# Performance work log

Hardware: AMD Instinct MI355X
Metric: run time of the kernel (lower is better)

## Reference

```python
import jax, jax.numpy as jnp
import numpy as np

D_MODEL = 512
D_INNER = 1024   # expand=2
D_STATE = 16
D_CONV = 4
DT_RANK = 32     # ceil(d_model/16)
B, L = 2, 2048


def _params(kbase):
    kk = jax.random.split(kbase, 9)
    n = lambda k, s, sc: jax.random.normal(k, s, jnp.float32) * sc
    return dict(
        Win=n(kk[0], (2 * D_INNER, D_MODEL), D_MODEL ** -0.5),
        convw=n(kk[1], (D_INNER, 1, D_CONV), 0.2),
        convb=n(kk[2], (D_INNER,), 0.02),
        Wx=n(kk[3], (DT_RANK + 2 * D_STATE, D_INNER), D_INNER ** -0.5),
        Wdt=n(kk[4], (D_INNER, DT_RANK), DT_RANK ** -0.5),
        dtb=n(kk[5], (D_INNER,), 0.1),
        Alog=n(kk[6], (D_INNER, D_STATE), 0.5),
        Dp=n(kk[7], (D_INNER,), 1.0),
        Wout=n(kk[8], (D_MODEL, D_INNER), D_INNER ** -0.5),
    )


def setup_inputs() -> dict:
    key = jax.random.key(0)
    k0, kf, kr = jax.random.split(key, 3)
    inp = {"hidden_states": jax.random.normal(k0, (B, L, D_MODEL), jnp.float32)}
    for name, v in _params(kf).items():
        inp[name + "_f"] = v
    for name, v in _params(kr).items():
        inp[name + "_r"] = v
    return inp


def _mamba(x, Win, convw, convb, Wx, Wdt, dtb, Alog, Dp, Wout):
    # x: (B, L, D_MODEL)
    Bb = x.shape[0]
    xz = jnp.einsum('bld,ed->ble', x, Win)            # (B, L, 2*D_INNER)
    xs, z = jnp.split(xz, 2, axis=-1)
    # causal depthwise conv over length
    xc = jnp.swapaxes(xs, 1, 2)                       # (B, D_INNER, L)
    xc = jax.lax.conv_general_dilated(
        xc, convw, (1,), [(D_CONV - 1, 0)], feature_group_count=D_INNER)
    xs = jax.nn.silu(jnp.swapaxes(xc + convb[None, :, None], 1, 2))  # (B, L, D_INNER)
    # input-dependent SSM params
    x_dbl = jnp.einsum('bld,ed->ble', xs, Wx)         # (B, L, DT_RANK+2*D_STATE)
    dt = x_dbl[..., :DT_RANK]
    Bm = x_dbl[..., DT_RANK:DT_RANK + D_STATE]        # (B, L, D_STATE)
    Cm = x_dbl[..., DT_RANK + D_STATE:]               # (B, L, D_STATE)
    dt = jax.nn.softplus(jnp.einsum('blr,dr->bld', dt, Wdt) + dtb)   # (B, L, D_INNER)
    A = -jnp.exp(Alog)                                # (D_INNER, D_STATE), strictly negative
    dA = jnp.exp(dt[..., None] * A)                   # (B, L, D_INNER, D_STATE)
    dBu = dt[..., None] * Bm[:, :, None, :] * xs[..., None]

    def step(h, inp):
        dA_t, dBu_t, C_t = inp
        h = dA_t * h + dBu_t                          # (B, D_INNER, D_STATE)
        return h, jnp.einsum('bds,bs->bd', h, C_t)

    h0 = jnp.zeros((Bb, D_INNER, D_STATE), x.dtype)
    _, ys = jax.lax.scan(
        step, h0,
        (jnp.moveaxis(dA, 1, 0), jnp.moveaxis(dBu, 1, 0), jnp.moveaxis(Cm, 1, 0)))
    y = jnp.moveaxis(ys, 0, 1) + xs * Dp              # (B, L, D_INNER)
    y = y * jax.nn.silu(z)                            # gated output
    return jnp.einsum('bld,ed->ble', y, Wout)         # (B, L, D_MODEL)


def reference(hidden_states,
              Win_f, convw_f, convb_f, Wx_f, Wdt_f, dtb_f, Alog_f, Dp_f, Wout_f,
              Win_r, convw_r, convb_r, Wx_r, Wdt_r, dtb_r, Alog_r, Dp_r, Wout_r):
    out_f = _mamba(hidden_states, Win_f, convw_f, convb_f, Wx_f, Wdt_f, dtb_f,
                   Alog_f, Dp_f, Wout_f)
    out_r = _mamba(hidden_states[:, ::-1, :], Win_r, convw_r, convb_r, Wx_r,
                   Wdt_r, dtb_r, Alog_r, Dp_r, Wout_r)[:, ::-1, :]
    return out_f + out_r  # bidirectional_strategy == 'add'
```

## Files before the change

### kernel.cpp

```cpp
#include <hip/hip_runtime.h>
#include <cmath>

#define B_   2
#define L_   2048
#define DM_  512
#define DI_  1024
#define DS_  16
#define DTR_ 32
#define M_   (B_*L_)
#define NC_  64
#define CL_  32
#define KS_  8
#define LOG2E_ 1.44269504088896340736f
#define LN2_   0.69314718055994530942f

typedef __attribute__((ext_vector_type(8))) short short8;
typedef __attribute__((ext_vector_type(4))) float floatx4;

__device__ inline unsigned short f2bf(float f) {
  unsigned u = __float_as_uint(f);
  unsigned r = (u + 0x7fffu + ((u >> 16) & 1u)) >> 16;
  return (unsigned short)r;
}
__device__ inline float bf2f(unsigned short u) {
  return __uint_as_float(((unsigned)u) << 16);
}
__device__ inline unsigned short f2h(float f) {
  _Float16 h = (_Float16)f;
  return *(unsigned short*)&h;
}
__device__ inline float h2f(unsigned short u) {
  _Float16 h = *(_Float16*)&u;
  return (float)h;
}
__device__ inline float fexp2(float x) { return __builtin_amdgcn_exp2f(x); }
__device__ inline float flog2(float x) { return __builtin_amdgcn_logf(x); }

__device__ inline void gload_lds16(const unsigned short* g, unsigned short* l) {
  __builtin_amdgcn_global_load_lds(
      (const __attribute__((address_space(1))) void*)g,
      (__attribute__((address_space(3))) void*)l, 16, 0, 0);
}

__global__ __launch_bounds__(256) void gemm1_mfma_k(
    const unsigned short* __restrict__ A,
    const unsigned short* __restrict__ Wf, const unsigned short* __restrict__ Wr,
    unsigned short* __restrict__ Cf, unsigned short* __restrict__ Cr,
    int M, int N, int K)
{
  __shared__ unsigned short At[2][128 * 32];
  __shared__ unsigned short Wt[2][128 * 32];
  const unsigned short* W = blockIdx.z ? Wr : Wf;
  unsigned short* C = blockIdx.z ? Cr : Cf;
  const int tid  = threadIdx.x;
  const int w    = tid >> 6;
  const int lane = tid & 63;
  const int wm   = w >> 1, wn = w & 1;
  const int row0 = blockIdx.y * 128, col0 = blockIdx.x * 128;
  const int lrow  = lane >> 2;
  const int lkoff = (lane & 3) * 8;
  const int fr = lane & 15;
  const int fq = (lane >> 4) * 8;

  floatx4 acc[4][4];
#pragma unroll
  for (int i = 0; i < 4; ++i)
#pragma unroll
    for (int j = 0; j < 4; ++j)
#pragma unroll
      for (int r = 0; r < 4; ++r) acc[i][j][r] = 0.f;

  auto stage = [&](int buf, int k0) {
#pragma unroll
    for (int j = 0; j < 2; ++j) {
      int r = w * 32 + j * 16;
      gload_lds16(A + (size_t)(row0 + r + lrow) * K + k0 + lkoff, At[buf] + r * 32);
      gload_lds16(W + (size_t)(col0 + r + lrow) * K + k0 + lkoff, Wt[buf] + r * 32);
    }
  };
  auto compute = [&](int buf) {
    short8 af[4], bf[4];
#pragma unroll
    for (int i = 0; i < 4; ++i) {
      af[i] = *(const short8*)&At[buf][(64 * wm + 16 * i + fr) * 32 + fq];
      bf[i] = *(const short8*)&Wt[buf][(64 * wn + 16 * i + fr) * 32 + fq];
    }
#pragma unroll
    for (int i = 0; i < 4; ++i)
#pragma unroll
      for (int j = 0; j < 4; ++j)
        acc[i][j] = __builtin_amdgcn_mfma_f32_16x16x32_bf16(af[i], bf[j], acc[i][j], 0, 0, 0);
  };

  const int NT = K >> 5;
  stage(0, 0);
  __syncthreads();
  int cur = 0;
  for (int t = 0; t < NT - 1; ++t) {
    stage(cur ^ 1, (t + 1) << 5);
    compute(cur);
    __syncthreads();
    cur ^= 1;
  }
  compute(cur);

#pragma unroll
  for (int i = 0; i < 4; ++i) {
    int rg = row0 + 64 * wm + 16 * i + ((lane >> 4) << 2);
#pragma unroll
    for (int j = 0; j < 4; ++j) {
      int cg = col0 + 64 * wn + 16 * j + (lane & 15);
#pragma unroll
      for (int r = 0; r < 4; ++r)
        C[(size_t)(rg + r) * N + cg] = f2bf(acc[i][j][r]);
    }
  }
}

__global__ __launch_bounds__(256) void gemm4_fused_k(
    const unsigned short* __restrict__ ybf, const unsigned short* __restrict__ Woutbf,
    const unsigned short* __restrict__ ybr, const unsigned short* __restrict__ Woutbr,
    float* __restrict__ out)
{
  __shared__ unsigned short At[2][2][64 * 32];
  __shared__ unsigned short Wt[2][2][64 * 32];
  const int tid  = threadIdx.x;
  const int w    = tid >> 6;
  const int lane = tid & 63;
  const int col0 = blockIdx.x * 64;
  const int row0 = blockIdx.y * 64;
  const int lrow  = lane >> 2;
  const int lkoff = (lane & 3) * 8;
  const int fr = lane & 15;
  const int fq = (lane >> 4) * 8;

  floatx4 acc[4];
#pragma unroll
  for (int j = 0; j < 4; ++j)
#pragma unroll
    for (int r = 0; r < 4; ++r) acc[j][r] = 0.f;

  auto stage = [&](int buf, int t) {
    const unsigned short* A = (t & 16) ? ybr : ybf;
    const unsigned short* W = (t & 16) ? Woutbr : Woutbf;
    const int k0 = (t & 15) << 6;
#pragma unroll
    for (int h = 0; h < 2; ++h) {
      gload_lds16(A + (size_t)(row0 + 16 * w + lrow) * DI_ + k0 + 32 * h + lkoff,
                  At[buf][h] + (16 * w) * 32);
      gload_lds16(W + (size_t)(col0 + 16 * w + lrow) * DI_ + k0 + 32 * h + lkoff,
                  Wt[buf][h] + (16 * w) * 32);
    }
  };
  auto compute = [&](int buf) {
    short8 af[2], bf[2][4];
#pragma unroll
    for (int h = 0; h < 2; ++h) {
      af[h] = *(const short8*)&At[buf][h][(16 * w + fr) * 32 + fq];
#pragma unroll
      for (int j = 0; j < 4; ++j)
        bf[h][j] = *(const short8*)&Wt[buf][h][(16 * j + fr) * 32 + fq];
    }
#pragma unroll
    for (int h = 0; h < 2; ++h)
#pragma unroll
      for (int j = 0; j < 4; ++j)
        acc[j] = __builtin_amdgcn_mfma_f32_16x16x32_bf16(af[h], bf[h][j], acc[j], 0, 0, 0);
  };

  stage(0, 0);
  __syncthreads();
  int cur = 0;
  for (int t = 0; t < 31; ++t) {
    stage(cur ^ 1, t + 1);
    compute(cur);
    __syncthreads();
    cur ^= 1;
  }
  compute(cur);

  const int rg = row0 + 16 * w + ((lane >> 4) << 2);
#pragma unroll
  for (int j = 0; j < 4; ++j) {
    int cg = col0 + 16 * j + (lane & 15);
#pragma unroll
    for (int r = 0; r < 4; ++r)
      out[(size_t)(rg + r) * DM_ + cg] = acc[j][r];
  }
}

__global__ __launch_bounds__(256) void gemm2_mfma_k(
    const unsigned short* __restrict__ xsbf, const unsigned short* __restrict__ xsbr,
    const unsigned short* __restrict__ Wxbf, const unsigned short* __restrict__ Wxbr,
    float* __restrict__ part)
{
  __shared__ unsigned short At[2][128 * 32];
  __shared__ unsigned short Wt[2][64 * 32];
  const int tid  = threadIdx.x;
  const int w    = tid >> 6;
  const int lane = tid & 63;
  const int ks   = blockIdx.x;
  const int row0 = blockIdx.y * 128;
  const int dir  = blockIdx.z;
  const unsigned short* A = dir ? xsbr : xsbf;
  const unsigned short* W = dir ? Wxbr : Wxbf;
  const int kbase = ks * (DI_ / KS_);
  const int lrow  = lane >> 2;
  const int lkoff = (lane & 3) * 8;
  const int fr = lane & 15;
  const int fq = (lane >> 4) * 8;

  floatx4 acc[2][4];
#pragma unroll
  for (int i = 0; i < 2; ++i)
#pragma unroll
    for (int j = 0; j < 4; ++j)
#pragma unroll
      for (int r = 0; r < 4; ++r) acc[i][j][r] = 0.f;

  auto stage = [&](int buf, int k0) {
#pragma unroll
    for (int j = 0; j < 2; ++j) {
      int r = w * 32 + j * 16;
      gload_lds16(A + (size_t)(row0 + r + lrow) * DI_ + kbase + k0 + lkoff, At[buf] + r * 32);
    }
    int r = w * 16;
    gload_lds16(W + (size_t)(r + lrow) * DI_ + kbase + k0 + lkoff, Wt[buf] + r * 32);
  };
  auto compute = [&](int buf) {
    short8 af[2], bf[4];
#pragma unroll
    for (int i = 0; i < 2; ++i)
      af[i] = *(const short8*)&At[buf][(32 * w + 16 * i + fr) * 32 + fq];
#pragma unroll
    for (int j = 0; j < 4; ++j)
      bf[j] = *(const short8*)&Wt[buf][(16 * j + fr) * 32 + fq];
#pragma unroll
    for (int i = 0; i < 2; ++i)
#pragma unroll
      for (int j = 0; j < 4; ++j)
        acc[i][j] = __builtin_amdgcn_mfma_f32_16x16x32_bf16(af[i], bf[j], acc[i][j], 0, 0, 0);
  };

  const int NT = (DI_ / KS_) >> 5;
  stage(0, 0);
  __syncthreads();
  int cur = 0;
  for (int t = 0; t < NT - 1; ++t) {
    stage(cur ^ 1, (t + 1) << 5);
    compute(cur);
    __syncthreads();
    cur ^= 1;
  }
  compute(cur);

  float* dst = part + (((size_t)dir * KS_ + ks) * M_) * 64;
#pragma unroll
  for (int i = 0; i < 2; ++i) {
    int rg = row0 + 32 * w + 16 * i + ((lane >> 4) << 2);
#pragma unroll
    for (int j = 0; j < 4; ++j) {
      int cg = 16 * j + (lane & 15);
#pragma unroll
      for (int r = 0; r < 4; ++r)
        dst[(size_t)(rg + r) * 64 + cg] = acc[i][j][r];
    }
  }
}

__global__ __launch_bounds__(256) void reduce_part_k(
    const float* __restrict__ part, float* __restrict__ xdf, float* __restrict__ xdr,
    unsigned short* __restrict__ drbf, unsigned short* __restrict__ drbr)
{
  int g = blockIdx.x * 256 + threadIdx.x;
  int n4  = g & 15;
  int m   = (g >> 4) & (M_ - 1);
  int dir = g >> 16;
  const float* p = part + ((size_t)dir * KS_ * M_ + m) * 64 + n4 * 4;
  float4 s = make_float4(0.f, 0.f, 0.f, 0.f);
#pragma unroll
  for (int ks = 0; ks < KS_; ++ks) {
    float4 v = *(const float4*)(p + (size_t)ks * M_ * 64);
    s.x += v.x; s.y += v.y; s.z += v.z; s.w += v.w;
  }
  float* xd = dir ? xdr : xdf;
  *(float4*)(xd + (size_t)m * 64 + n4 * 4) = s;
  if (n4 < 8) {
    unsigned short* dr = dir ? drbr : drbf;
    ushort4 o;
    o.x = f2bf(s.x); o.y = f2bf(s.y); o.z = f2bf(s.z); o.w = f2bf(s.w);
    *(ushort4*)(dr + (size_t)m * 32 + n4 * 4) = o;
  }
}

struct CastArgs {
  const float* src[9];
  unsigned short* dst[9];
  int start[9];
  int n[9];
};

__global__ __launch_bounds__(256) void cast_multi_k(
    CastArgs a, int total4,
    const float* __restrict__ Alf, const float* __restrict__ Alr,
    float* __restrict__ Atf, float* __restrict__ Atr)
{
  int g = blockIdx.x * 256 + threadIdx.x;
  if (g >= total4) return;
  if (g < 8192) {
    const float* Al = (g < 4096) ? Alf : Alr;
    float* At = (g < 4096) ? Atf : Atr;
    int off = (g & 4095) * 4;
    float4 v = *(const float4*)(Al + off);
    float4 o = make_float4(-__expf(v.x) * LOG2E_, -__expf(v.y) * LOG2E_,
                           -__expf(v.z) * LOG2E_, -__expf(v.w) * LOG2E_);
    *(float4*)(At + off) = o;
  }
  int e = g * 4;
#pragma unroll 1
  for (int s = 0; s < 9; ++s) {
    if (e < a.start[s] + a.n[s]) {
      int off = e - a.start[s];
      float4 v = *(const float4*)(a.src[s] + off);
      ushort4 o;
      o.x = f2bf(v.x); o.y = f2bf(v.y); o.z = f2bf(v.z); o.w = f2bf(v.w);
      *(ushort4*)(a.dst[s] + off) = o;
      return;
    }
  }
}

__global__ __launch_bounds__(256) void gemm3_mfma_k(
    const unsigned short* __restrict__ drbf, const unsigned short* __restrict__ drbr,
    const unsigned short* __restrict__ Wdtbf, const unsigned short* __restrict__ Wdtbr,
    const float* __restrict__ b0, const float* __restrict__ b1,
    unsigned short* __restrict__ C0, unsigned short* __restrict__ C1)
{
  __shared__ unsigned short At[128 * 32];
  __shared__ unsigned short Wt[128 * 32];
  const unsigned short* A = blockIdx.z ? drbr : drbf;
  const unsigned short* W = blockIdx.z ? Wdtbr : Wdtbf;
  const float* bias = blockIdx.z ? b1 : b0;
  unsigned short* C = blockIdx.z ? C1 : C0;
  const int tid  = threadIdx.x;
  const int w    = tid >> 6;
  const int lane = tid & 63;
  const int wm   = w >> 1, wn = w & 1;
  const int row0 = blockIdx.y * 128, col0 = blockIdx.x * 128;
  const int lrow  = lane >> 2;
  const int lkoff = (lane & 3) * 8;
  const int fr = lane & 15;
  const int fq = (lane >> 4) * 8;

#pragma unroll
  for (int j = 0; j < 2; ++j) {
    int r = w * 32 + j * 16;
    gload_lds16(A + (size_t)(row0 + r + lrow) * DTR_ + lkoff, At + r * 32);
    gload_lds16(W + (size_t)(col0 + r + lrow) * DTR_ + lkoff, Wt + r * 32);
  }
  __syncthreads();
  short8 af[4], bf[4];
#pragma unroll
  for (int i = 0; i < 4; ++i) {
    af[i] = *(const short8*)&At[(64 * wm + 16 * i + fr) * 32 + fq];
    bf[i] = *(const short8*)&Wt[(64 * wn + 16 * i + fr) * 32 + fq];
  }
  floatx4 acc[4][4];
#pragma unroll
  for (int i = 0; i < 4; ++i)
#pragma unroll
    for (int j = 0; j < 4; ++j) {
#pragma unroll
      for (int r = 0; r < 4; ++r) acc[i][j][r] = 0.f;
      acc[i][j] = __builtin_amdgcn_mfma_f32_16x16x32_bf16(af[i], bf[j], acc[i][j], 0, 0, 0);
    }
#pragma unroll
  for (int i = 0; i < 4; ++i) {
    int rg = row0 + 64 * wm + 16 * i + ((lane >> 4) << 2);
#pragma unroll
    for (int j = 0; j < 4; ++j) {
      int cg = col0 + 64 * wn + 16 * j + (lane & 15);
      float bv = bias[cg];
#pragma unroll
      for (int r = 0; r < 4; ++r) {
        float v = acc[i][j][r] + bv;
        float e = fexp2(-fabsf(v) * LOG2E_);
        float sp = fmaxf(v, 0.f) + LN2_ * flog2(1.f + e);
        C[(size_t)(rg + r) * DI_ + cg] = f2h(sp);
      }
    }
  }
}

__global__ __launch_bounds__(256) void conv_silu_k(
    const unsigned short* __restrict__ xzbf, const unsigned short* __restrict__ xzbr,
    const float* __restrict__ cwf, const float* __restrict__ cbf,
    const float* __restrict__ cwr, const float* __restrict__ cbr,
    unsigned short* __restrict__ xsbf, unsigned short* __restrict__ xsbr)
{
  int bid = blockIdx.x;
  int t   = bid & (L_ - 1);
  int b   = (bid >> 11) & (B_ - 1);
  int dir = bid >> 12;
  const unsigned short* xz = dir ? xzbr : xzbf;
  const float* cw = dir ? cwr : cwf;
  const float* cb = dir ? cbr : cbf;
  unsigned short* xsb = dir ? xsbr : xsbf;
  int d0 = threadIdx.x << 2;
  float wv[4][4];
#pragma unroll
  for (int i = 0; i < 4; ++i) {
    float4 w4 = *(const float4*)(cw + (size_t)(d0 + i) * 4);
    wv[i][0] = w4.x; wv[i][1] = w4.y; wv[i][2] = w4.z; wv[i][3] = w4.w;
  }
  float4 cbv = *(const float4*)(cb + d0);
  float acc[4] = {cbv.x, cbv.y, cbv.z, cbv.w};
#pragma unroll
  for (int j = 0; j < 4; ++j) {
    int tt = dir ? (t + 3 - j) : (t - 3 + j);
    if (tt >= 0 && tt < L_) {
      ushort4 v = *(const ushort4*)(xz + ((size_t)b * L_ + tt) * 2048 + d0);
      acc[0] = fmaf(wv[0][j], bf2f(v.x), acc[0]);
      acc[1] = fmaf(wv[1][j], bf2f(v.y), acc[1]);
      acc[2] = fmaf(wv[2][j], bf2f(v.z), acc[2]);
      acc[3] = fmaf(wv[3][j], bf2f(v.w), acc[3]);
    }
  }
  float4 o;
  o.x = acc[0] * __builtin_amdgcn_rcpf(1.f + fexp2(-acc[0] * LOG2E_));
  o.y = acc[1] * __builtin_amdgcn_rcpf(1.f + fexp2(-acc[1] * LOG2E_));
  o.z = acc[2] * __builtin_amdgcn_rcpf(1.f + fexp2(-acc[2] * LOG2E_));
  o.w = acc[3] * __builtin_amdgcn_rcpf(1.f + fexp2(-acc[3] * LOG2E_));
  ushort4 ob;
  ob.x = f2bf(o.x); ob.y = f2bf(o.y); ob.z = f2bf(o.z); ob.w = f2bf(o.w);
  *(ushort4*)(xsb + ((size_t)b * L_ + t) * DI_ + d0) = ob;
}

__global__ __launch_bounds__(256) void scan_passA_k(
    const unsigned short* __restrict__ dtf, const unsigned short* __restrict__ dtr,
    const unsigned short* __restrict__ xsbf, const unsigned short* __restrict__ xsbr,
    const float* __restrict__ xdf, const float* __restrict__ xdr,
    const float* __restrict__ Atabf, const float* __restrict__ Atabr,
    float* __restrict__ E, float* __restrict__ dts)
{
  __shared__ float bS[CL_][16];
  int bid  = blockIdx.x;
  int dgrp = bid & 3;
  int c    = (bid >> 2) & (NC_ - 1);
  int b    = (bid >> 8) & 1;
  int dir  = bid >> 9;
  int d    = (dgrp << 8) + threadIdx.x;
  const unsigned short* dt = dir ? dtr : dtf;
  const unsigned short* xs = dir ? xsbr : xsbf;
  const float* xd = dir ? xdr : xdf;
  const float* At = dir ? Atabr : Atabf;
  if (threadIdx.x < CL_ * 4) {
    int li = threadIdx.x >> 2;
    int lc = threadIdx.x & 3;
    *(float4*)&bS[li][lc * 4] =
        *(const float4*)(xd + ((size_t)b * L_ + c * CL_ + li) * 64 + 32 + lc * 4);
  }
  float Ai2[16];
#pragma unroll
  for (int q = 0; q < 4; ++q) {
    float4 a4 = *(const float4*)(At + (size_t)d * 16 + q * 4);
    Ai2[4*q] = a4.x; Ai2[4*q+1] = a4.y; Ai2[4*q+2] = a4.z; Ai2[4*q+3] = a4.w;
  }
  float h[16];
#pragma unroll
  for (int s = 0; s < 16; ++s) h[s] = 0.f;
  int t0 = c * CL_ + (dir ? CL_ - 1 : 0);
  const long sdt = (dir ? -1L : 1L) * DI_;
  const unsigned short* dtp = dt + ((size_t)b * L_ + t0) * DI_ + d;
  const unsigned short* xsp = xs + ((size_t)b * L_ + t0) * DI_ + d;
  float dtsum = 0.f;
  __syncthreads();
#pragma unroll 2
  for (int i = 0; i < CL_; ++i) {
    int row = dir ? (CL_ - 1 - i) : i;
    float dtv = h2f(*dtp);
    float xv  = bf2f(*xsp);
    float Bv[16];
#pragma unroll
    for (int q = 0; q < 4; ++q) {
      float4 bq = *(const float4*)&bS[row][4 * q];
      Bv[4*q] = bq.x; Bv[4*q+1] = bq.y; Bv[4*q+2] = bq.z; Bv[4*q+3] = bq.w;
    }
    float dtx = dtv * xv;
    dtsum += dtv;
#pragma unroll
    for (int s = 0; s < 16; ++s) {
      float dA = fexp2(dtv * Ai2[s]);
      h[s] = fmaf(dA, h[s], dtx * Bv[s]);
    }
    dtp += sdt; xsp += sdt;
  }
  size_t base = ((((size_t)dir * B_ + b) * NC_ + c) * DI_ + d) * 16;
#pragma unroll
  for (int q = 0; q < 4; ++q)
    *(float4*)(E + base + q * 4) = make_float4(h[4*q], h[4*q+1], h[4*q+2], h[4*q+3]);
  dts[(((size_t)dir * B_ + b) * NC_ + c) * DI_ + d] = dtsum;
}

__global__ __launch_bounds__(256) void scan_prefix_k(
    const float* __restrict__ E, const float* __restrict__ dts,
    const float* __restrict__ Atabf, const float* __restrict__ Atabr,
    float* __restrict__ Hin)
{
  int gid = blockIdx.x * 256 + threadIdx.x;
  int s   = gid & 15;
  int d   = (gid >> 4) & (DI_ - 1);
  int b   = (gid >> 14) & 1;
  int dir = gid >> 15;
  float Ai2 = (dir ? Atabr : Atabf)[(size_t)d * 16 + s];
  size_t eb  = (((size_t)dir * B_ + b) * NC_) * DI_ * 16 + (size_t)d * 16 + s;
  size_t db2 = (((size_t)dir * B_ + b) * NC_) * DI_ + d;
  const long es = (long)DI_ * 16;
  float h = 0.f;
  if (!dir) {
    size_t idx = eb;
    size_t di  = db2;
    float Ec = E[idx], dc = dts[di];
#pragma unroll 2
    for (int c = 0; c < NC_ - 1; ++c) {
      float En = E[idx + es];
      float dn = dts[di + DI_];
      Hin[idx] = h;
      h = fmaf(fexp2(dc * Ai2), h, Ec);
      Ec = En; dc = dn; idx += es; di += DI_;
    }
    Hin[idx] = h;
  } else {
    size_t idx = eb + (size_t)(NC_ - 1) * es;
    size_t di  = db2 + (size_t)(NC_ - 1) * DI_;
    float Ec = E[idx], dc = dts[di];
#pragma unroll 2
    for (int c = 0; c < NC_ - 1; ++c) {
      float En = E[idx - es];
      float dn = dts[di - DI_];
      Hin[idx] = h;
      h = fmaf(fexp2(dc * Ai2), h, Ec);
      Ec = En; dc = dn; idx -= es; di -= DI_;
    }
    Hin[idx] = h;
  }
}

__global__ __launch_bounds__(256) void scan_passC_k(
    const unsigned short* __restrict__ dtf, const unsigned short* __restrict__ dtr,
    const unsigned short* __restrict__ xsbf, const unsigned short* __restrict__ xsbr,
    const float* __restrict__ xdf, const float* __restrict__ xdr,
    const unsigned short* __restrict__ xzbf, const unsigned short* __restrict__ xzbr,
    const float* __restrict__ Atabf, const float* __restrict__ Atabr,
    const float* __restrict__ Dpf, const float* __restrict__ Dpr,
    const float* __restrict__ Hin,
    unsigned short* __restrict__ ybf, unsigned short* __restrict__ ybr)
{
  __shared__ float bcS[CL_][32];
  int bid  = blockIdx.x;
  int dgrp = bid & 3;
  int c    = (bid >> 2) & (NC_ - 1);
  int b    = (bid >> 8) & 1;
  int dir  = bid >> 9;
  int d    = (dgrp << 8) + threadIdx.x;
  const unsigned short* dt  = dir ? dtr : dtf;
  const unsigned short* xs = dir ? xsbr : xsbf;
  const float* xd  = dir ? xdr : xdf;
  const unsigned short* xz = dir ? xzbr : xzbf;
  const float* At  = dir ? Atabr : Atabf;
  unsigned short* yb = dir ? ybr : ybf;
  float Dpv = (dir ? Dpr : Dpf)[d];
  {
    int li = threadIdx.x >> 3;
    int lc = threadIdx.x & 7;
    *(float4*)&bcS[li][lc * 4] =
        *(const float4*)(xd + ((size_t)b * L_ + c * CL_ + li) * 64 + 32 + lc * 4);
  }
  float Ai2[16];
#pragma unroll
  for (int q = 0; q < 4; ++q) {
    float4 a4 = *(const float4*)(At + (size_t)d * 16 + q * 4);
    Ai2[4*q] = a4.x; Ai2[4*q+1] = a4.y; Ai2[4*q+2] = a4.z; Ai2[4*q+3] = a4.w;
  }
  size_t hb = ((((size_t)dir * B_ + b) * NC_ + c) * DI_ + d) * 16;
  float h[16];
#pragma unroll
  for (int q = 0; q < 4; ++q) {
    float4 hv = *(const float4*)(Hin + hb + q * 4);
    h[4*q] = hv.x; h[4*q+1] = hv.y; h[4*q+2] = hv.z; h[4*q+3] = hv.w;
  }
  int t0 = c * CL_ + (dir ? CL_ - 1 : 0);
  const long sdt = (dir ? -1L : 1L) * DI_;
  const long sz_ = (dir ? -1L : 1L) * 2048;
  const unsigned short* dtp = dt + ((size_t)b * L_ + t0) * DI_ + d;
  const unsigned short* xsp = xs + ((size_t)b * L_ + t0) * DI_ + d;
  const unsigned short* zp = xz + ((size_t)b * L_ + t0) * 2048 + DI_ + d;
  unsigned short* ybp = yb + ((size_t)b * L_ + t0) * DI_ + d;
  __syncthreads();
#pragma unroll 2
  for (int i = 0; i < CL_; ++i) {
    int row = dir ? (CL_ - 1 - i) : i;
    float dtv = h2f(*dtp);
    float xv  = bf2f(*xsp);
    float z   = bf2f(*zp);
    float Bv[16], Cv[16];
#pragma unroll
    for (int q = 0; q < 4; ++q) {
      float4 bq = *(const float4*)&bcS[row][4 * q];
      float4 cq = *(const float4*)&bcS[row][16 + 4 * q];
      Bv[4*q] = bq.x; Bv[4*q+1] = bq.y; Bv[4*q+2] = bq.z; Bv[4*q+3] = bq.w;
      Cv[4*q] = cq.x; Cv[4*q+1] = cq.y; Cv[4*q+2] = cq.z; Cv[4*q+3] = cq.w;
    }
    float dtx = dtv * xv;
    float yacc = 0.f;
#pragma unroll
    for (int s = 0; s < 16; ++s) {
      float dA = fexp2(dtv * Ai2[s]);
      h[s] = fmaf(dA, h[s], dtx * Bv[s]);
      yacc = fmaf(h[s], Cv[s], yacc);
    }
    float yv = fmaf(xv, Dpv, yacc);
    float sz = z * __builtin_amdgcn_rcpf(1.f + fexp2(-z * LOG2E_));
    *ybp = f2bf(yv * sz);
    dtp += sdt; xsp += sdt; zp += sz_; ybp += sdt;
  }
}

extern "C" void kernel_launch(void* const* d_in, const int* in_sizes, int n_in,
                              void* d_out, int out_size, void* d_ws, size_t ws_size,
                              hipStream_t stream)
{
  const float* x       = (const float*)d_in[0];
  const float* Win_f   = (const float*)d_in[1];
  const float* convw_f = (const float*)d_in[2];
  const float* convb_f = (const float*)d_in[3];
  const float* Wx_f    = (const float*)d_in[4];
  const float* Wdt_f   = (const float*)d_in[5];
  const float* dtb_f   = (const float*)d_in[6];
  const float* Alog_f  = (const float*)d_in[7];
  const float* Dp_f    = (const float*)d_in[8];
  const float* Wout_f  = (const float*)d_in[9];
  const float* Win_r   = (const float*)d_in[10];
  const float* convw_r = (const float*)d_in[11];
  const float* convb_r = (const float*)d_in[12];
  const float* Wx_r    = (const float*)d_in[13];
  const float* Wdt_r   = (const float*)d_in[14];
  const float* dtb_r   = (const float*)d_in[15];
  const float* Alog_r  = (const float*)d_in[16];
  const float* Dp_r    = (const float*)d_in[17];
  const float* Wout_r  = (const float*)d_in[18];
  float* out = (float*)d_out;

  float* ws  = (float*)d_ws;
  float* xdf = ws;
  float* xdr = xdf + (size_t)M_ * 64;
  unsigned short* dtf = (unsigned short*)(xdr + (size_t)M_ * 64);
  unsigned short* dtr = dtf + (size_t)M_ * DI_;
  float* Eb  = (float*)(dtr + (size_t)M_ * DI_);
  float* Hb  = Eb + (size_t)2 * B_ * NC_ * DI_ * 16;
  float* dtsb = Hb + (size_t)2 * B_ * NC_ * DI_ * 16;
  float* part2 = Eb;
  unsigned short* xzbf    = (unsigned short*)(dtsb + (size_t)2 * B_ * NC_ * DI_);
  unsigned short* xzbr    = xzbf + (size_t)M_ * 2048;
  unsigned short* xb      = xzbr + (size_t)M_ * 2048;
  unsigned short* Winb_f  = xb + (size_t)M_ * DM_;
  unsigned short* Winb_r  = Winb_f + (size_t)2048 * DM_;
  unsigned short* Woutb_f = Winb_r + (size_t)2048 * DM_;
  unsigned short* Woutb_r = Woutb_f + (size_t)DM_ * DI_;
  unsigned short* ybf     = Woutb_r + (size_t)DM_ * DI_;
  unsigned short* ybr     = ybf + (size_t)M_ * DI_;
  unsigned short* xsbf    = ybr + (size_t)M_ * DI_;
  unsigned short* xsbr    = xsbf + (size_t)M_ * DI_;
  unsigned short* Wxb_f   = xsbr + (size_t)M_ * DI_;
  unsigned short* Wxb_r   = Wxb_f + (size_t)64 * DI_;
  unsigned short* Wdtb_f  = Wxb_r + (size_t)64 * DI_;
  unsigned short* Wdtb_r  = Wdtb_f + (size_t)DI_ * DTR_;
  unsigned short* drbf    = Wdtb_r + (size_t)DI_ * DTR_;
  unsigned short* drbr    = drbf + (size_t)M_ * DTR_;
  float* Atabf = (float*)(drbr + (size_t)M_ * DTR_);
  float* Atabr = Atabf + (size_t)DI_ * DS_;

  dim3 blk(256);

  {
    CastArgs ca;
    ca.src[0] = x;      ca.dst[0] = xb;      ca.n[0] = M_ * DM_;
    ca.src[1] = Win_f;  ca.dst[1] = Winb_f;  ca.n[1] = 2048 * DM_;
    ca.src[2] = Win_r;  ca.dst[2] = Winb_r;  ca.n[2] = 2048 * DM_;
    ca.src[3] = Wout_f; ca.dst[3] = Woutb_f; ca.n[3] = DM_ * DI_;
    ca.src[4] = Wout_r; ca.dst[4] = Woutb_r; ca.n[4] = DM_ * DI_;
    ca.src[5] = Wx_f;   ca.dst[5] = Wxb_f;   ca.n[5] = 64 * DI_;
    ca.src[6] = Wx_r;   ca.dst[6] = Wxb_r;   ca.n[6] = 64 * DI_;
    ca.src[7] = Wdt_f;  ca.dst[7] = Wdtb_f;  ca.n[7] = DI_ * DTR_;
    ca.src[8] = Wdt_r;  ca.dst[8] = Wdtb_r;  ca.n[8] = DI_ * DTR_;
    int st = 0;
    for (int s = 0; s < 9; ++s) { ca.start[s] = st; st += ca.n[s]; }
    int total4 = st / 4;
    cast_multi_k<<<(total4 + 255) / 256, blk, 0, stream>>>(
        ca, total4, Alog_f, Alog_r, Atabf, Atabr);
  }

  gemm1_mfma_k<<<dim3(2048 / 128, M_ / 128, 2), blk, 0, stream>>>(
      xb, Winb_f, Winb_r, xzbf, xzbr, M_, 2048, DM_);

  conv_silu_k<<<2 * B_ * L_, blk, 0, stream>>>(xzbf, xzbr, convw_f, convb_f,
      convw_r, convb_r, xsbf, xsbr);

  gemm2_mfma_k<<<dim3(KS_, M_ / 128, 2), blk, 0, stream>>>(
      xsbf, xsbr, Wxb_f, Wxb_r, part2);
  reduce_part_k<<<(2 * M_ * 16) / 256, blk, 0, stream>>>(part2, xdf, xdr,
      drbf, drbr);

  gemm3_mfma_k<<<dim3(DI_ / 128, M_ / 128, 2), blk, 0, stream>>>(
      drbf, drbr, Wdtb_f, Wdtb_r, dtb_f, dtb_r, dtf, dtr);

  scan_passA_k<<<2 * B_ * NC_ * 4, blk, 0, stream>>>(dtf, dtr, xsbf, xsbr,
      xdf, xdr, Atabf, Atabr, Eb, dtsb);
  scan_prefix_k<<<(2 * B_ * DI_ * 16) / 256, blk, 0, stream>>>(
      Eb, dtsb, Atabf, Atabr, Hb);
  scan_passC_k<<<2 * B_ * NC_ * 4, blk, 0, stream>>>(dtf, dtr, xsbf, xsbr,
      xdf, xdr, xzbf, xzbr, Atabf, Atabr, Dp_f, Dp_r, Hb, ybf, ybr);

  gemm4_fused_k<<<dim3(DM_ / 64, M_ / 64), blk, 0, stream>>>(
      ybf, Woutb_f, ybr, Woutb_r, out);
}
```

Baseline: 272.3 us.

## Fuse forward/reverse in-proj GEMMs sharing A tile; conv computes two timesteps

The input-projection GEMM now computes both the forward and reverse weight products in one block, loading the shared activation tile once and keeping two accumulator sets. The depthwise conv kernel processes two adjacent timesteps per block, reusing the overlapping input rows. This aims to cut redundant global loads of the activation tile and the conv inputs. The cost is doubled accumulator registers in the GEMM, with possible spills or lower occupancy, and half as many blocks.

Measured after the change: 261.0 us. 4.1% less time.

```diff
diff --git a/kernel.cpp b/kernel.cpp
--- a/kernel.cpp
+++ b/kernel.cpp
@@ -42,16 +42,15 @@
       (__attribute__((address_space(3))) void*)l, 16, 0, 0);
 }
 
-__global__ __launch_bounds__(256) void gemm1_mfma_k(
+__global__ __launch_bounds__(256, 2) void gemm1_mfma_k(
     const unsigned short* __restrict__ A,
     const unsigned short* __restrict__ Wf, const unsigned short* __restrict__ Wr,
     unsigned short* __restrict__ Cf, unsigned short* __restrict__ Cr,
-    int M, int N, int K)
+    int N, int K)
 {
   __shared__ unsigned short At[2][128 * 32];
-  __shared__ unsigned short Wt[2][128 * 32];
-  const unsigned short* W = blockIdx.z ? Wr : Wf;
-  unsigned short* C = blockIdx.z ? Cr : Cf;
+  __shared__ unsigned short Wtf[2][128 * 32];
+  __shared__ unsigned short Wtr[2][128 * 32];
   const int tid  = threadIdx.x;
   const int w    = tid >> 6;
   const int lane = tid & 63;
@@ -62,34 +61,38 @@
   const int fr = lane & 15;
   const int fq = (lane >> 4) * 8;
 
-  floatx4 acc[4][4];
+  floatx4 accf[4][4], accr[4][4];
 #pragma unroll
   for (int i = 0; i < 4; ++i)
 #pragma unroll
     for (int j = 0; j < 4; ++j)
 #pragma unroll
-      for (int r = 0; r < 4; ++r) acc[i][j][r] = 0.f;
+      for (int r = 0; r < 4; ++r) { accf[i][j][r] = 0.f; accr[i][j][r] = 0.f; }
 
   auto stage = [&](int buf, int k0) {
 #pragma unroll
     for (int j = 0; j < 2; ++j) {
       int r = w * 32 + j * 16;
-      gload_lds16(A + (size_t)(row0 + r + lrow) * K + k0 + lkoff, At[buf] + r * 32);
-      gload_lds16(W + (size_t)(col0 + r + lrow) * K + k0 + lkoff, Wt[buf] + r * 32);
+      gload_lds16(A  + (size_t)(row0 + r + lrow) * K + k0 + lkoff, At[buf]  + r * 32);
+      gload_lds16(Wf + (size_t)(col0 + r + lrow) * K + k0 + lkoff, Wtf[buf] + r * 32);
+      gload_lds16(Wr + (size_t)(col0 + r + lrow) * K + k0 + lkoff, Wtr[buf] + r * 32);
     }
   };
   auto compute = [&](int buf) {
-    short8 af[4], bf[4];
+    short8 af[4], bff[4], bfr[4];
 #pragma unroll
     for (int i = 0; i < 4; ++i) {
-      af[i] = *(const short8*)&At[buf][(64 * wm + 16 * i + fr) * 32 + fq];
-      bf[i] = *(const short8*)&Wt[buf][(64 * wn + 16 * i + fr) * 32 + fq];
+      af[i]  = *(const short8*)&At[buf][(64 * wm + 16 * i + fr) * 32 + fq];
+      bff[i] = *(const short8*)&Wtf[buf][(64 * wn + 16 * i + fr) * 32 + fq];
+      bfr[i] = *(const short8*)&Wtr[buf][(64 * wn + 16 * i + fr) * 32 + fq];
     }
 #pragma unroll
     for (int i = 0; i < 4; ++i)
 #pragma unroll
-      for (int j = 0; j < 4; ++j)
-        acc[i][j] = __builtin_amdgcn_mfma_f32_16x16x32_bf16(af[i], bf[j], acc[i][j], 0, 0, 0);
+      for (int j = 0; j < 4; ++j) {
+        accf[i][j] = __builtin_amdgcn_mfma_f32_16x16x32_bf16(af[i], bff[j], accf[i][j], 0, 0, 0);
+        accr[i][j] = __builtin_amdgcn_mfma_f32_16x16x32_bf16(af[i], bfr[j], accr[i][j], 0, 0, 0);
+      }
   };
 
   const int NT = K >> 5;
@@ -111,8 +114,10 @@
     for (int j = 0; j < 4; ++j) {
       int cg = col0 + 64 * wn + 16 * j + (lane & 15);
 #pragma unroll
-      for (int r = 0; r < 4; ++r)
-        C[(size_t)(rg + r) * N + cg] = f2bf(acc[i][j][r]);
+      for (int r = 0; r < 4; ++r) {
+        Cf[(size_t)(rg + r) * N + cg] = f2bf(accf[i][j][r]);
+        Cr[(size_t)(rg + r) * N + cg] = f2bf(accr[i][j][r]);
+      }
     }
   }
 }
@@ -399,9 +404,10 @@
     unsigned short* __restrict__ xsbf, unsigned short* __restrict__ xsbr)
 {
   int bid = blockIdx.x;
-  int t   = bid & (L_ - 1);
-  int b   = (bid >> 11) & (B_ - 1);
-  int dir = bid >> 12;
+  int t2  = bid & (L_ / 2 - 1);
+  int b   = (bid >> 10) & (B_ - 1);
+  int dir = bid >> 11;
+  int t   = t2 << 1;
   const unsigned short* xz = dir ? xzbr : xzbf;
   const float* cw = dir ? cwr : cwf;
   const float* cb = dir ? cbr : cbf;
@@ -414,26 +420,40 @@
     wv[i][0] = w4.x; wv[i][1] = w4.y; wv[i][2] = w4.z; wv[i][3] = w4.w;
   }
   float4 cbv = *(const float4*)(cb + d0);
-  float acc[4] = {cbv.x, cbv.y, cbv.z, cbv.w};
-#pragma unroll
-  for (int j = 0; j < 4; ++j) {
-    int tt = dir ? (t + 3 - j) : (t - 3 + j);
+  float accA[4] = {cbv.x, cbv.y, cbv.z, cbv.w};
+  float accB[4] = {cbv.x, cbv.y, cbv.z, cbv.w};
+#pragma unroll
+  for (int j = 0; j < 5; ++j) {
+    int tt = dir ? (t + 4 - j) : (t - 3 + j);
     if (tt >= 0 && tt < L_) {
       ushort4 v = *(const ushort4*)(xz + ((size_t)b * L_ + tt) * 2048 + d0);
-      acc[0] = fmaf(wv[0][j], bf2f(v.x), acc[0]);
-      acc[1] = fmaf(wv[1][j], bf2f(v.y), acc[1]);
-      acc[2] = fmaf(wv[2][j], bf2f(v.z), acc[2]);
-      acc[3] = fmaf(wv[3][j], bf2f(v.w), acc[3]);
-    }
-  }
-  float4 o;
-  o.x = acc[0] * __builtin_amdgcn_rcpf(1.f + fexp2(-acc[0] * LOG2E_));
-  o.y = acc[1] * __builtin_amdgcn_rcpf(1.f + fexp2(-acc[1] * LOG2E_));
-  o.z = acc[2] * __builtin_amdgcn_rcpf(1.f + fexp2(-acc[2] * LOG2E_));
-  o.w = acc[3] * __builtin_amdgcn_rcpf(1.f + fexp2(-acc[3] * LOG2E_));
-  ushort4 ob;
-  ob.x = f2bf(o.x); ob.y = f2bf(o.y); ob.z = f2bf(o.z); ob.w = f2bf(o.w);
-  *(ushort4*)(xsb + ((size_t)b * L_ + t) * DI_ + d0) = ob;
+      float f0 = bf2f(v.x), f1 = bf2f(v.y), f2 = bf2f(v.z), f3 = bf2f(v.w);
+      if (j < 4) {
+        accA[0] = fmaf(wv[0][j], f0, accA[0]);
+        accA[1] = fmaf(wv[1][j], f1, accA[1]);
+        accA[2] = fmaf(wv[2][j], f2, accA[2]);
+        accA[3] = fmaf(wv[3][j], f3, accA[3]);
+      }
+      if (j >= 1) {
+        accB[0] = fmaf(wv[0][j - 1], f0, accB[0]);
+        accB[1] = fmaf(wv[1][j - 1], f1, accB[1]);
+        accB[2] = fmaf(wv[2][j - 1], f2, accB[2]);
+        accB[3] = fmaf(wv[3][j - 1], f3, accB[3]);
+      }
+    }
+  }
+  int tA = dir ? t + 1 : t;
+  int tB = dir ? t : t + 1;
+  ushort4 oa, ob;
+#pragma unroll
+  for (int i = 0; i < 4; ++i) {
+    float sa = accA[i] * __builtin_amdgcn_rcpf(1.f + fexp2(-accA[i] * LOG2E_));
+    float sb = accB[i] * __builtin_amdgcn_rcpf(1.f + fexp2(-accB[i] * LOG2E_));
+    ((unsigned short*)&oa)[i] = f2bf(sa);
+    ((unsigned short*)&ob)[i] = f2bf(sb);
+  }
+  *(ushort4*)(xsb + ((size_t)b * L_ + tA) * DI_ + d0) = oa;
+  *(ushort4*)(xsb + ((size_t)b * L_ + tB) * DI_ + d0) = ob;
 }
 
 __global__ __launch_bounds__(256) void scan_passA_k(
@@ -700,10 +720,10 @@
         ca, total4, Alog_f, Alog_r, Atabf, Atabr);
   }
 
-  gemm1_mfma_k<<<dim3(2048 / 128, M_ / 128, 2), blk, 0, stream>>>(
-      xb, Winb_f, Winb_r, xzbf, xzbr, M_, 2048, DM_);
-
-  conv_silu_k<<<2 * B_ * L_, blk, 0, stream>>>(xzbf, xzbr, convw_f, convb_f,
+  gemm1_mfma_k<<<dim3(2048 / 128, M_ / 128), blk, 0, stream>>>(
+      xb, Winb_f, Winb_r, xzbf, xzbr, 2048, DM_);
+
+  conv_silu_k<<<2 * B_ * (L_ / 2), blk, 0, stream>>>(xzbf, xzbr, convw_f, convb_f,
       convw_r, convb_r, xsbf, xsbr);
 
   gemm2_mfma_k<<<dim3(KS_, M_ / 128, 2), blk, 0, stream>>>(
```
